# Kernel optimization log

Hardware: AMD Instinct MI355X
Metric: run time of the kernel (lower is better)

Reference implementation:

```python
import jax, jax.numpy as jnp
import numpy as np

N_NODES = 100000
N_EDGES = 400000
D_IN = 128
D_OUT = 128
BN_EPS = 1e-5


def setup_inputs() -> dict:
    key = jax.random.key(0)
    ks = jax.random.split(key, 9)
    node_feats = jax.random.normal(ks[0], (N_NODES, D_IN), dtype=jnp.float32)
    src = jax.random.randint(ks[1], (N_EDGES,), 0, N_NODES)
    dst = jax.random.randint(ks[2], (N_EDGES,), 0, N_NODES)
    # GraphConv weight/bias
    W = jax.random.normal(ks[3], (D_IN, D_OUT), dtype=jnp.float32) * (1.0 / np.sqrt(D_IN))
    b = jax.random.normal(ks[4], (D_OUT,), dtype=jnp.float32) * 0.01
    # residual Linear weight/bias
    Wr = jax.random.normal(ks[5], (D_IN, D_OUT), dtype=jnp.float32) * (1.0 / np.sqrt(D_IN))
    br = jax.random.normal(ks[6], (D_OUT,), dtype=jnp.float32) * 0.01
    # BatchNorm1d affine params
    gamma = jnp.ones((D_OUT,), dtype=jnp.float32) + 0.1 * jax.random.normal(ks[7], (D_OUT,), dtype=jnp.float32)
    beta = 0.1 * jax.random.normal(ks[8], (D_OUT,), dtype=jnp.float32)
    return {"node_feats": node_feats, "W": W, "b": b, "Wr": Wr, "br": br,
            "gamma": gamma, "beta": beta, "src": src, "dst": dst}


def reference(node_feats, W, b, Wr, br, gamma, beta, src, dst):
    ones_e = jnp.ones((src.shape[0],), dtype=node_feats.dtype)
    out_deg = jax.ops.segment_sum(ones_e, src, num_segments=N_NODES)
    in_deg = jax.ops.segment_sum(ones_e, dst, num_segments=N_NODES)
    # norm='both': D_out^{-1/2} on source side, D_in^{-1/2} on dest side (clamp 0-degree)
    c_src = jax.lax.rsqrt(jnp.maximum(out_deg, 1.0))  # [N]
    c_dst = jax.lax.rsqrt(jnp.maximum(in_deg, 1.0))   # [N]
    x_scaled = node_feats * c_src[:, None]            # [N, D_in]
    msgs = x_scaled[src]                              # gather -> [E, D_in]
    agg = jax.ops.segment_sum(msgs, dst, num_segments=N_NODES)  # scatter-add -> [N, D_in]
    h = agg * c_dst[:, None]
    h = jax.nn.relu(h @ W + b)                        # GraphConv activation
    res = jax.nn.relu(node_feats @ Wr + br)           # residual branch
    y = h + res
    # BatchNorm1d, training mode: batch stats, biased variance
    mean = jnp.mean(y, axis=0)
    var = jnp.mean(jnp.square(y - mean), axis=0)
    y_hat = (y - mean) * jax.lax.rsqrt(var + BN_EPS)
    return y_hat * gamma + beta
```

## Files before the change

kernel.cpp:

```cpp
#include <hip/hip_runtime.h>

#define N_NODES 100000
#define N_EDGES 400000
#define D 128
#define BN_EPS 1e-5f
#define NTILES 6250

typedef short short8 __attribute__((ext_vector_type(8)));
typedef float f32x4 __attribute__((ext_vector_type(4)));

static __device__ __forceinline__ float bf2f(unsigned short u) {
    unsigned x = ((unsigned)u) << 16;
    return __builtin_bit_cast(float, x);
}
static __device__ __forceinline__ unsigned short f2bf(float f) {
    unsigned x = __builtin_bit_cast(unsigned, f);
    x += 0x7fffu + ((x >> 16) & 1u);
    return (unsigned short)(x >> 16);
}
static __device__ __forceinline__ void splitbf(float a, short& hi, short& lo) {
    unsigned short h = f2bf(a);
    float r = a - bf2f(h);
    hi = (short)h;
    lo = (short)f2bf(r);
}
static __device__ __forceinline__ void split2(float a, float b, unsigned& hiw, unsigned& low) {
    short ha, la, hb, lb;
    splitbf(a, ha, la);
    splitbf(b, hb, lb);
    hiw = (unsigned)(unsigned short)ha | ((unsigned)(unsigned short)hb << 16);
    low = (unsigned)(unsigned short)la | ((unsigned)(unsigned short)lb << 16);
}
static __device__ __forceinline__ void split8(f32x4 a, f32x4 b, uint4& hi, uint4& lo) {
    unsigned h0, h1, h2, h3, l0, l1, l2, l3;
    split2(a[0], a[1], h0, l0);
    split2(a[2], a[3], h1, l1);
    split2(b[0], b[1], h2, l2);
    split2(b[2], b[3], h3, l3);
    hi = uint4{h0, h1, h2, h3};
    lo = uint4{l0, l1, l2, l3};
}

__global__ void k_zero_out(float* __restrict__ y, int n4) {
    int t = blockIdx.x * blockDim.x + threadIdx.x;
    if (t < n4) ((float4*)y)[t] = float4{0.f, 0.f, 0.f, 0.f};
}

__global__ void k_count(const int* __restrict__ src, const int* __restrict__ dst,
                        int* __restrict__ cnt_src, int* __restrict__ cnt_dst) {
    int t = blockIdx.x * blockDim.x + threadIdx.x;
    if (t >= N_EDGES) return;
    atomicAdd(&cnt_src[src[t]], 1);
    atomicAdd(&cnt_dst[dst[t]], 1);
}

__global__ void k_coeffs(const int* __restrict__ cnt_src, const int* __restrict__ cnt_dst,
                         float* __restrict__ c_src, float* __restrict__ c_dst,
                         int* __restrict__ fill) {
    int t = blockIdx.x * blockDim.x + threadIdx.x;
    if (t >= N_NODES) return;
    c_src[t] = rsqrtf(fmaxf((float)cnt_src[t], 1.0f));
    c_dst[t] = rsqrtf(fmaxf((float)cnt_dst[t], 1.0f));
    fill[t] = 0;
}

__global__ void k_scan1(const int* __restrict__ cnt, int* __restrict__ outp,
                        int* __restrict__ bsum) {
    __shared__ int s[256];
    int i = blockIdx.x * 256 + threadIdx.x;
    int v = (i < N_NODES) ? cnt[i] : 0;
    s[threadIdx.x] = v;
    __syncthreads();
    for (int d = 1; d < 256; d <<= 1) {
        int t = (threadIdx.x >= d) ? s[threadIdx.x - d] : 0;
        __syncthreads();
        s[threadIdx.x] += t;
        __syncthreads();
    }
    if (i < N_NODES) outp[i] = s[threadIdx.x] - v;
    if (threadIdx.x == 255) bsum[blockIdx.x] = s[255];
}

__global__ void k_scan2(int* __restrict__ bsum, int nb) {
    __shared__ int s[512];
    int v = (threadIdx.x < nb) ? bsum[threadIdx.x] : 0;
    s[threadIdx.x] = v;
    __syncthreads();
    for (int d = 1; d < 512; d <<= 1) {
        int t = (threadIdx.x >= d) ? s[threadIdx.x - d] : 0;
        __syncthreads();
        s[threadIdx.x] += t;
        __syncthreads();
    }
    if (threadIdx.x < nb) bsum[threadIdx.x] = s[threadIdx.x] - v;
}

__global__ void k_scan3(int* __restrict__ rowStart, const int* __restrict__ boff) {
    int i = blockIdx.x * 256 + threadIdx.x;
    if (i < N_NODES) rowStart[i] += boff[i >> 8];
    if (i == 0) rowStart[N_NODES] = N_EDGES;
}

__global__ void k_fill(const int* __restrict__ src, const int* __restrict__ dst,
                       const int* __restrict__ rowStart, int* __restrict__ fill,
                       int* __restrict__ esorted) {
    int e = blockIdx.x * blockDim.x + threadIdx.x;
    if (e >= N_EDGES) return;
    int d = dst[e];
    int pos = rowStart[d] + atomicAdd(&fill[d], 1);
    esorted[pos] = src[e];
}

__global__ void k_make_frags(const float* __restrict__ W,
                             const float* __restrict__ Wr,
                             unsigned short* __restrict__ Whi, unsigned short* __restrict__ Wlo,
                             unsigned short* __restrict__ Wrhi, unsigned short* __restrict__ Wrlo) {
    int t = blockIdx.x * blockDim.x + threadIdx.x;
    if (t >= 4096) return;
    int mat = t >> 11;
    int fragIdx = (t >> 6) & 31;
    int lane = t & 63;
    int nt = fragIdx >> 2, ks = fragIdx & 3;
    const float* Wsrc = mat ? Wr : W;
    unsigned short* dhi = mat ? Wrhi : Whi;
    unsigned short* dlo = mat ? Wrlo : Wlo;
    int n = nt * 16 + (lane & 15);
    int kbase = ks * 32 + (lane >> 4) * 8;
    short hi[8], lo[8];
#pragma unroll
    for (int j = 0; j < 8; j++) splitbf(Wsrc[(kbase + j) * D + n], hi[j], lo[j]);
    ((uint4*)dhi)[fragIdx * 64 + lane] = *(uint4*)hi;
    ((uint4*)dlo)[fragIdx * 64 + lane] = *(uint4*)lo;
}

__global__ __launch_bounds__(256, 2) void k_fused(
    const float* __restrict__ x,
    const int* __restrict__ esorted, const int* __restrict__ rowStart,
    const float* __restrict__ c_src, const float* __restrict__ c_dst,
    const unsigned short* __restrict__ Whi, const unsigned short* __restrict__ Wlo,
    const unsigned short* __restrict__ Wrhi, const unsigned short* __restrict__ Wrlo,
    const float* __restrict__ bias_h, const float* __restrict__ bias_r,
    float* __restrict__ yout,
    float* __restrict__ gsum, float* __restrict__ gsq) {
    __shared__ uint4 A[2][16][64];
    __shared__ float Y[4][16 * 36];

    const int wave = threadIdx.x >> 6;
    const int lane = threadIdx.x & 63;
    const int quad = lane >> 4;
    const int l16 = lane & 15;
    float* __restrict__ ldsY = &Y[wave][0];

    short8 wHf[8], wLf[8], rHf[8], rLf[8];
#pragma unroll
    for (int f = 0; f < 8; f++) {
        int nt = wave * 2 + (f >> 2), ks = f & 3;
        int gi = (nt * 4 + ks) * 64 + lane;
        wHf[f] = __builtin_bit_cast(short8, ((const uint4*)Whi)[gi]);
        wLf[f] = __builtin_bit_cast(short8, ((const uint4*)Wlo)[gi]);
        rHf[f] = __builtin_bit_cast(short8, ((const uint4*)Wrhi)[gi]);
        rLf[f] = __builtin_bit_cast(short8, ((const uint4*)Wrlo)[gi]);
    }
    float bh[2], brr[2];
#pragma unroll
    for (int ntl = 0; ntl < 2; ntl++) {
        int col = wave * 32 + ntl * 16 + l16;
        bh[ntl] = bias_h[col];
        brr[ntl] = bias_r[col];
    }

    float s_acc[2] = {0.f, 0.f}, q_acc[2] = {0.f, 0.f};
    const f32x4* __restrict__ xb = (const f32x4*)x;

    int buf = 0;
    for (int rt = blockIdx.x; rt < NTILES; rt += gridDim.x, buf ^= 1) {
        const int rowbase = rt * 16;

        {
            const int R = wave * 4 + quad;
            const int n = rowbase + R;
            const int li = l16;
            const int beg = rowStart[n], end = rowStart[n + 1];
            f32x4 X0 = xb[(size_t)n * 32 + li * 2], X1 = xb[(size_t)n * 32 + li * 2 + 1];
            f32x4 A0 = {0.f, 0.f, 0.f, 0.f}, A1 = {0.f, 0.f, 0.f, 0.f};
            for (int j = beg; j < end; j += 8) {
                int idx[8];
                float c[8];
                f32x4 pa[8], pb[8];
#pragma unroll
                for (int k = 0; k < 8; k++) {
                    int jj = j + k;
                    idx[k] = esorted[(jj < end) ? jj : j];
                }
#pragma unroll
                for (int k = 0; k < 8; k++)
                    c[k] = (j + k < end) ? c_src[idx[k]] : 0.f;
#pragma unroll
                for (int k = 0; k < 8; k++) {
                    pa[k] = xb[(size_t)idx[k] * 32 + li * 2];
                    pb[k] = xb[(size_t)idx[k] * 32 + li * 2 + 1];
                }
#pragma unroll
                for (int k = 0; k < 8; k++) {
                    A0 += pa[k] * c[k];
                    A1 += pb[k] * c[k];
                }
            }
            float cd = c_dst[n];
            A0 *= cd; A1 *= cd;
            uint4 ahi, alo, xhi, xlo;
            split8(A0, A1, ahi, alo);
            split8(X0, X1, xhi, xlo);
            uint4* Arow = &A[buf][R][0];
            const int sw = li ^ (R & 7);
            Arow[sw] = ahi;
            Arow[16 + sw] = alo;
            Arow[32 + sw] = xhi;
            Arow[48 + sw] = xlo;
        }
        __syncthreads();

        const uint4* rowA = &A[buf][l16][0];
        const int r7 = l16 & 7;
        short8 aH[4], aL[4], xH[4], xL[4];
#pragma unroll
        for (int ks = 0; ks < 4; ks++) {
            const int sl = (ks * 4 + quad) ^ r7;
            aH[ks] = __builtin_bit_cast(short8, rowA[sl]);
            aL[ks] = __builtin_bit_cast(short8, rowA[16 + sl]);
            xH[ks] = __builtin_bit_cast(short8, rowA[32 + sl]);
            xL[ks] = __builtin_bit_cast(short8, rowA[48 + sl]);
        }

        f32x4 accH[2], accR[2];
#pragma unroll
        for (int ntl = 0; ntl < 2; ntl++) {
            accH[ntl] = f32x4{0.f, 0.f, 0.f, 0.f};
            accR[ntl] = f32x4{0.f, 0.f, 0.f, 0.f};
#pragma unroll
            for (int ks = 0; ks < 4; ks++) {
                const int f = ntl * 4 + ks;
                accH[ntl] = __builtin_amdgcn_mfma_f32_16x16x32_bf16(aH[ks], wHf[f], accH[ntl], 0, 0, 0);
                accH[ntl] = __builtin_amdgcn_mfma_f32_16x16x32_bf16(aH[ks], wLf[f], accH[ntl], 0, 0, 0);
                accH[ntl] = __builtin_amdgcn_mfma_f32_16x16x32_bf16(aL[ks], wHf[f], accH[ntl], 0, 0, 0);
                accR[ntl] = __builtin_amdgcn_mfma_f32_16x16x32_bf16(xH[ks], rHf[f], accR[ntl], 0, 0, 0);
                accR[ntl] = __builtin_amdgcn_mfma_f32_16x16x32_bf16(xH[ks], rLf[f], accR[ntl], 0, 0, 0);
                accR[ntl] = __builtin_amdgcn_mfma_f32_16x16x32_bf16(xL[ks], rHf[f], accR[ntl], 0, 0, 0);
            }
        }

#pragma unroll
        for (int ntl = 0; ntl < 2; ntl++) {
            float s = 0.f, q = 0.f;
#pragma unroll
            for (int r = 0; r < 4; r++) {
                float y = fmaxf(accH[ntl][r] + bh[ntl], 0.f) + fmaxf(accR[ntl][r] + brr[ntl], 0.f);
                ldsY[(quad * 4 + r) * 36 + ntl * 16 + l16] = y;
                s += y;
                q += y * y;
            }
            s_acc[ntl] += s;
            q_acc[ntl] += q;
        }
        asm volatile("s_waitcnt lgkmcnt(0)");
#pragma unroll
        for (int j = 0; j < 2; j++) {
            int trow = j * 8 + (lane >> 3);
            int tc4 = lane & 7;
            float4 v = *(const float4*)&ldsY[trow * 36 + tc4 * 4];
            ((float4*)(yout + (size_t)(rowbase + trow) * D + wave * 32))[tc4] = v;
        }
    }

#pragma unroll
    for (int ntl = 0; ntl < 2; ntl++) {
        float s = s_acc[ntl], q = q_acc[ntl];
        s += __shfl_xor(s, 16, 64);
        s += __shfl_xor(s, 32, 64);
        q += __shfl_xor(q, 16, 64);
        q += __shfl_xor(q, 32, 64);
        if (lane < 16) {
            unsafeAtomicAdd(&gsum[wave * 32 + ntl * 16 + lane], s);
            unsafeAtomicAdd(&gsq[wave * 32 + ntl * 16 + lane], q);
        }
    }
}

__global__ void k_bn_stats(const float* __restrict__ gsum, const float* __restrict__ gsq,
                           const float* __restrict__ gamma, const float* __restrict__ beta,
                           float* __restrict__ scale, float* __restrict__ shift) {
    int f = threadIdx.x;
    const float invN = 1.0f / (float)N_NODES;
    float mean = gsum[f] * invN;
    float var = fmaxf(gsq[f] * invN - mean * mean, 0.f);
    float sc = gamma[f] * rsqrtf(var + BN_EPS);
    scale[f] = sc;
    shift[f] = beta[f] - mean * sc;
}

__global__ void k_bn_apply(float* __restrict__ y,
                           const float* __restrict__ scale, const float* __restrict__ shift) {
    int t = blockIdx.x * blockDim.x + threadIdx.x;
    const int total4 = N_NODES * D / 4;
    if (t >= total4) return;
    float4 v = ((float4*)y)[t];
    int f = (t * 4) & (D - 1);
    v.x = v.x * scale[f] + shift[f];
    v.y = v.y * scale[f + 1] + shift[f + 1];
    v.z = v.z * scale[f + 2] + shift[f + 2];
    v.w = v.w * scale[f + 3] + shift[f + 3];
    ((float4*)y)[t] = v;
}

extern "C" void kernel_launch(void* const* d_in, const int* in_sizes, int n_in,
                              void* d_out, int out_size, void* d_ws, size_t ws_size,
                              hipStream_t stream) {
    const float* x     = (const float*)d_in[0];
    const float* W     = (const float*)d_in[1];
    const float* b     = (const float*)d_in[2];
    const float* Wr    = (const float*)d_in[3];
    const float* br    = (const float*)d_in[4];
    const float* gamma = (const float*)d_in[5];
    const float* beta  = (const float*)d_in[6];
    const int* src = (const int*)d_in[7];
    const int* dst = (const int*)d_in[8];
    float* out = (float*)d_out;

    const int NB1 = (N_NODES + 255) / 256;

    char* ws = (char*)d_ws;
    size_t off = 0;
    float* gsum    = (float*)(ws + off); off += 512;
    float* gsq     = (float*)(ws + off); off += 512;
    int* cnt_src   = (int*)(ws + off); off += 400128;
    int* cnt_dst   = (int*)(ws + off); off += 400128;
    const size_t zero_bytes = off;
    int* fill      = (int*)(ws + off); off += 400128;
    int* rowStart  = (int*)(ws + off); off += 400384;
    int* bsum      = (int*)(ws + off); off += 2048;
    int* esorted   = (int*)(ws + off); off += (size_t)N_EDGES * 4;
    float* c_src   = (float*)(ws + off); off += 400128;
    float* c_dst   = (float*)(ws + off); off += 400128;
    unsigned short* WhiF  = (unsigned short*)(ws + off); off += 32768;
    unsigned short* WloF  = (unsigned short*)(ws + off); off += 32768;
    unsigned short* WrhiF = (unsigned short*)(ws + off); off += 32768;
    unsigned short* WrloF = (unsigned short*)(ws + off); off += 32768;
    float* scale = (float*)(ws + off); off += 512;
    float* shift = (float*)(ws + off); off += 512;
    const size_t needed = off;

    if (ws_size < needed) {
        k_zero_out<<<(N_NODES * D / 4 + 255) / 256, 256, 0, stream>>>(out, N_NODES * D / 4);
        return;
    }

    hipMemsetAsync(d_ws, 0, zero_bytes, stream);

    k_make_frags<<<16, 256, 0, stream>>>(W, Wr, WhiF, WloF, WrhiF, WrloF);
    k_count<<<(N_EDGES + 255) / 256, 256, 0, stream>>>(src, dst, cnt_src, cnt_dst);
    k_coeffs<<<NB1, 256, 0, stream>>>(cnt_src, cnt_dst, c_src, c_dst, fill);
    k_scan1<<<NB1, 256, 0, stream>>>(cnt_dst, rowStart, bsum);
    k_scan2<<<1, 512, 0, stream>>>(bsum, NB1);
    k_scan3<<<NB1, 256, 0, stream>>>(rowStart, bsum);
    k_fill<<<(N_EDGES + 255) / 256, 256, 0, stream>>>(src, dst, rowStart, fill, esorted);
    k_fused<<<1024, 256, 0, stream>>>(x, esorted, rowStart, c_src, c_dst,
                                      WhiF, WloF, WrhiF, WrloF, b, br, out, gsum, gsq);
    k_bn_stats<<<1, 128, 0, stream>>>(gsum, gsq, gamma, beta, scale, shift);
    k_bn_apply<<<(N_NODES * D / 4 + 255) / 256, 256, 0, stream>>>(out, scale, shift);
}
```

Before: 250.5 us.

## Software-pipeline gather under MFMA and fold BatchNorm into cooperative kernel

Restructures the fused kernel so each tile's neighbour gather for the next row tile is issued in stages between the GraphConv and residual MFMA blocks. This hides global-load latency behind matrix math. The BN statistics and apply steps move into the same kernel behind a cooperative grid sync, which removes two launches but halves the grid to 512 blocks and re-reads the output. The coefficient kernel is also merged into the first scan pass. The cooperative launch needs a fallback path, and the smaller grid may lower occupancy for the gather.

```diff
diff --git a/kernel.cpp b/kernel.cpp
--- a/kernel.cpp
+++ b/kernel.cpp
@@ -1,10 +1,12 @@
 #include <hip/hip_runtime.h>
+#include <hip/hip_cooperative_groups.h>
 
 #define N_NODES 100000
 #define N_EDGES 400000
 #define D 128
 #define BN_EPS 1e-5f
 #define NTILES 6250
+#define COOP_GRID 512
 
 typedef short short8 __attribute__((ext_vector_type(8)));
 typedef float f32x4 __attribute__((ext_vector_type(4)));
@@ -54,21 +56,19 @@
     atomicAdd(&cnt_dst[dst[t]], 1);
 }
 
-__global__ void k_coeffs(const int* __restrict__ cnt_src, const int* __restrict__ cnt_dst,
-                         float* __restrict__ c_src, float* __restrict__ c_dst,
-                         int* __restrict__ fill) {
-    int t = blockIdx.x * blockDim.x + threadIdx.x;
-    if (t >= N_NODES) return;
-    c_src[t] = rsqrtf(fmaxf((float)cnt_src[t], 1.0f));
-    c_dst[t] = rsqrtf(fmaxf((float)cnt_dst[t], 1.0f));
-    fill[t] = 0;
-}
-
 __global__ void k_scan1(const int* __restrict__ cnt, int* __restrict__ outp,
-                        int* __restrict__ bsum) {
+                        int* __restrict__ bsum,
+                        const int* __restrict__ cnt_src,
+                        float* __restrict__ c_src, float* __restrict__ c_dst,
+                        int* __restrict__ fill) {
     __shared__ int s[256];
     int i = blockIdx.x * 256 + threadIdx.x;
     int v = (i < N_NODES) ? cnt[i] : 0;
+    if (i < N_NODES) {
+        c_src[i] = rsqrtf(fmaxf((float)cnt_src[i], 1.0f));
+        c_dst[i] = rsqrtf(fmaxf((float)v, 1.0f));
+        fill[i] = 0;
+    }
     s[threadIdx.x] = v;
     __syncthreads();
     for (int d = 1; d < 256; d <<= 1) {
@@ -141,15 +141,21 @@
     const unsigned short* __restrict__ Wrhi, const unsigned short* __restrict__ Wrlo,
     const float* __restrict__ bias_h, const float* __restrict__ bias_r,
     float* __restrict__ yout,
-    float* __restrict__ gsum, float* __restrict__ gsq) {
+    float* __restrict__ gsum, float* __restrict__ gsq,
+    const float* __restrict__ gamma, const float* __restrict__ beta,
+    int coop) {
     __shared__ uint4 A[2][16][64];
     __shared__ float Y[4][16 * 36];
+    __shared__ float sc[128], sh[128];
 
     const int wave = threadIdx.x >> 6;
     const int lane = threadIdx.x & 63;
     const int quad = lane >> 4;
     const int l16 = lane & 15;
+    const int R = wave * 4 + quad;
+    const int li = l16;
     float* __restrict__ ldsY = &Y[wave][0];
+    const f32x4* __restrict__ xb = (const f32x4*)x;
 
     short8 wHf[8], wLf[8], rHf[8], rLf[8];
 #pragma unroll
@@ -170,55 +176,64 @@
     }
 
     float s_acc[2] = {0.f, 0.f}, q_acc[2] = {0.f, 0.f};
-    const f32x4* __restrict__ xb = (const f32x4*)x;
+    const int rt0 = blockIdx.x;
+    const int G = gridDim.x;
+
+    {
+        const int n = rt0 * 16 + R;
+        const int beg = rowStart[n], end = rowStart[n + 1];
+        f32x4 X0 = xb[(size_t)n * 32 + li * 2], X1 = xb[(size_t)n * 32 + li * 2 + 1];
+        f32x4 A0 = {0.f, 0.f, 0.f, 0.f}, A1 = {0.f, 0.f, 0.f, 0.f};
+        for (int j = beg; j < end; j += 8) {
+            int idx[8]; float c[8]; f32x4 pa[8], pb[8];
+#pragma unroll
+            for (int k = 0; k < 8; k++) {
+                int jj = j + k;
+                idx[k] = esorted[(jj < end) ? jj : j];
+            }
+#pragma unroll
+            for (int k = 0; k < 8; k++) c[k] = (j + k < end) ? c_src[idx[k]] : 0.f;
+#pragma unroll
+            for (int k = 0; k < 8; k++) {
+                pa[k] = xb[(size_t)idx[k] * 32 + li * 2];
+                pb[k] = xb[(size_t)idx[k] * 32 + li * 2 + 1];
+            }
+#pragma unroll
+            for (int k = 0; k < 8; k++) { A0 += pa[k] * c[k]; A1 += pb[k] * c[k]; }
+        }
+        float cd = c_dst[n];
+        A0 *= cd; A1 *= cd;
+        uint4 ahi, alo, xhi, xlo;
+        split8(A0, A1, ahi, alo);
+        split8(X0, X1, xhi, xlo);
+        uint4* Arow = &A[0][R][0];
+        const int sw = li ^ (R & 7);
+        Arow[sw] = ahi; Arow[16 + sw] = alo; Arow[32 + sw] = xhi; Arow[48 + sw] = xlo;
+    }
+    int beg1 = 0, end1 = 0;
+    if (rt0 + G < NTILES) {
+        int n1 = (rt0 + G) * 16 + R;
+        beg1 = rowStart[n1];
+        end1 = rowStart[n1 + 1];
+    }
 
     int buf = 0;
-    for (int rt = blockIdx.x; rt < NTILES; rt += gridDim.x, buf ^= 1) {
+    for (int rt = rt0; rt < NTILES; rt += G, buf ^= 1) {
         const int rowbase = rt * 16;
-
-        {
-            const int R = wave * 4 + quad;
-            const int n = rowbase + R;
-            const int li = l16;
-            const int beg = rowStart[n], end = rowStart[n + 1];
-            f32x4 X0 = xb[(size_t)n * 32 + li * 2], X1 = xb[(size_t)n * 32 + li * 2 + 1];
-            f32x4 A0 = {0.f, 0.f, 0.f, 0.f}, A1 = {0.f, 0.f, 0.f, 0.f};
-            for (int j = beg; j < end; j += 8) {
-                int idx[8];
-                float c[8];
-                f32x4 pa[8], pb[8];
-#pragma unroll
-                for (int k = 0; k < 8; k++) {
-                    int jj = j + k;
-                    idx[k] = esorted[(jj < end) ? jj : j];
-                }
-#pragma unroll
-                for (int k = 0; k < 8; k++)
-                    c[k] = (j + k < end) ? c_src[idx[k]] : 0.f;
-#pragma unroll
-                for (int k = 0; k < 8; k++) {
-                    pa[k] = xb[(size_t)idx[k] * 32 + li * 2];
-                    pb[k] = xb[(size_t)idx[k] * 32 + li * 2 + 1];
-                }
-#pragma unroll
-                for (int k = 0; k < 8; k++) {
-                    A0 += pa[k] * c[k];
-                    A1 += pb[k] * c[k];
-                }
-            }
-            float cd = c_dst[n];
-            A0 *= cd; A1 *= cd;
-            uint4 ahi, alo, xhi, xlo;
-            split8(A0, A1, ahi, alo);
-            split8(X0, X1, xhi, xlo);
-            uint4* Arow = &A[buf][R][0];
-            const int sw = li ^ (R & 7);
-            Arow[sw] = ahi;
-            Arow[16 + sw] = alo;
-            Arow[32 + sw] = xhi;
-            Arow[48 + sw] = xlo;
-        }
-        __syncthreads();
+        const int rtn = rt + G;
+        const bool pf = rtn < NTILES;
+        const int n1 = rtn * 16 + R;
+
+        __syncthreads();
+
+        int idx[8];
+        if (pf) {
+#pragma unroll
+            for (int k = 0; k < 8; k++) {
+                int jj = beg1 + k;
+                idx[k] = esorted[(jj < end1) ? jj : beg1];
+            }
+        }
 
         const uint4* rowA = &A[buf][l16][0];
         const int r7 = l16 & 7;
@@ -236,17 +251,42 @@
 #pragma unroll
         for (int ntl = 0; ntl < 2; ntl++) {
             accH[ntl] = f32x4{0.f, 0.f, 0.f, 0.f};
-            accR[ntl] = f32x4{0.f, 0.f, 0.f, 0.f};
 #pragma unroll
             for (int ks = 0; ks < 4; ks++) {
                 const int f = ntl * 4 + ks;
                 accH[ntl] = __builtin_amdgcn_mfma_f32_16x16x32_bf16(aH[ks], wHf[f], accH[ntl], 0, 0, 0);
                 accH[ntl] = __builtin_amdgcn_mfma_f32_16x16x32_bf16(aH[ks], wLf[f], accH[ntl], 0, 0, 0);
                 accH[ntl] = __builtin_amdgcn_mfma_f32_16x16x32_bf16(aL[ks], wHf[f], accH[ntl], 0, 0, 0);
+            }
+        }
+
+        float c[8];
+        if (pf) {
+#pragma unroll
+            for (int k = 0; k < 8; k++) c[k] = (beg1 + k < end1) ? c_src[idx[k]] : 0.f;
+        }
+
+#pragma unroll
+        for (int ntl = 0; ntl < 2; ntl++) {
+            accR[ntl] = f32x4{0.f, 0.f, 0.f, 0.f};
+#pragma unroll
+            for (int ks = 0; ks < 4; ks++) {
+                const int f = ntl * 4 + ks;
                 accR[ntl] = __builtin_amdgcn_mfma_f32_16x16x32_bf16(xH[ks], rHf[f], accR[ntl], 0, 0, 0);
                 accR[ntl] = __builtin_amdgcn_mfma_f32_16x16x32_bf16(xH[ks], rLf[f], accR[ntl], 0, 0, 0);
                 accR[ntl] = __builtin_amdgcn_mfma_f32_16x16x32_bf16(xL[ks], rHf[f], accR[ntl], 0, 0, 0);
             }
+        }
+
+        f32x4 pa[8], pb[8], X0n, X1n;
+        if (pf) {
+#pragma unroll
+            for (int k = 0; k < 8; k++) {
+                pa[k] = xb[(size_t)idx[k] * 32 + li * 2];
+                pb[k] = xb[(size_t)idx[k] * 32 + li * 2 + 1];
+            }
+            X0n = xb[(size_t)n1 * 32 + li * 2];
+            X1n = xb[(size_t)n1 * 32 + li * 2 + 1];
         }
 
 #pragma unroll
@@ -269,6 +309,43 @@
             int tc4 = lane & 7;
             float4 v = *(const float4*)&ldsY[trow * 36 + tc4 * 4];
             ((float4*)(yout + (size_t)(rowbase + trow) * D + wave * 32))[tc4] = v;
+        }
+
+        if (pf) {
+            f32x4 A0 = {0.f, 0.f, 0.f, 0.f}, A1 = {0.f, 0.f, 0.f, 0.f};
+#pragma unroll
+            for (int k = 0; k < 8; k++) { A0 += pa[k] * c[k]; A1 += pb[k] * c[k]; }
+            for (int j = beg1 + 8; j < end1; j += 8) {
+                int idx2[8]; float c2[8]; f32x4 qa[8], qb[8];
+#pragma unroll
+                for (int k = 0; k < 8; k++) {
+                    int jj = j + k;
+                    idx2[k] = esorted[(jj < end1) ? jj : j];
+                }
+#pragma unroll
+                for (int k = 0; k < 8; k++) c2[k] = (j + k < end1) ? c_src[idx2[k]] : 0.f;
+#pragma unroll
+                for (int k = 0; k < 8; k++) {
+                    qa[k] = xb[(size_t)idx2[k] * 32 + li * 2];
+                    qb[k] = xb[(size_t)idx2[k] * 32 + li * 2 + 1];
+                }
+#pragma unroll
+                for (int k = 0; k < 8; k++) { A0 += qa[k] * c2[k]; A1 += qb[k] * c2[k]; }
+            }
+            float cd = c_dst[n1];
+            A0 *= cd; A1 *= cd;
+            uint4 ahi, alo, xhi, xlo;
+            split8(A0, A1, ahi, alo);
+            split8(X0n, X1n, xhi, xlo);
+            uint4* Arow = &A[buf ^ 1][R][0];
+            const int sw = li ^ (R & 7);
+            Arow[sw] = ahi; Arow[16 + sw] = alo; Arow[32 + sw] = xhi; Arow[48 + sw] = xlo;
+            int rt2 = rtn + G;
+            if (rt2 < NTILES) {
+                int n2 = rt2 * 16 + R;
+                beg1 = rowStart[n2];
+                end1 = rowStart[n2 + 1];
+            }
         }
     }
 
@@ -282,6 +359,32 @@
         if (lane < 16) {
             unsafeAtomicAdd(&gsum[wave * 32 + ntl * 16 + lane], s);
             unsafeAtomicAdd(&gsq[wave * 32 + ntl * 16 + lane], q);
+        }
+    }
+
+    if (coop) {
+        cooperative_groups::this_grid().sync();
+        if (threadIdx.x < 128) {
+            int f = threadIdx.x;
+            float s = __hip_atomic_load(&gsum[f], __ATOMIC_RELAXED, __HIP_MEMORY_SCOPE_AGENT);
+            float q = __hip_atomic_load(&gsq[f], __ATOMIC_RELAXED, __HIP_MEMORY_SCOPE_AGENT);
+            const float invN = 1.0f / (float)N_NODES;
+            float mean = s * invN;
+            float var = fmaxf(q * invN - mean * mean, 0.f);
+            float scl = gamma[f] * rsqrtf(var + BN_EPS);
+            sc[f] = scl;
+            sh[f] = beta[f] - mean * scl;
+        }
+        __syncthreads();
+        const int total4 = N_NODES * D / 4;
+        for (int i = blockIdx.x * blockDim.x + threadIdx.x; i < total4; i += gridDim.x * blockDim.x) {
+            float4 v = ((float4*)yout)[i];
+            int f = (i * 4) & (D - 1);
+            v.x = v.x * sc[f] + sh[f];
+            v.y = v.y * sc[f + 1] + sh[f + 1];
+            v.z = v.z * sc[f + 2] + sh[f + 2];
+            v.w = v.w * sc[f + 3] + sh[f + 3];
+            ((float4*)yout)[i] = v;
         }
     }
 }
@@ -358,13 +461,26 @@
 
     k_make_frags<<<16, 256, 0, stream>>>(W, Wr, WhiF, WloF, WrhiF, WrloF);
     k_count<<<(N_EDGES + 255) / 256, 256, 0, stream>>>(src, dst, cnt_src, cnt_dst);
-    k_coeffs<<<NB1, 256, 0, stream>>>(cnt_src, cnt_dst, c_src, c_dst, fill);
-    k_scan1<<<NB1, 256, 0, stream>>>(cnt_dst, rowStart, bsum);
+    k_scan1<<<NB1, 256, 0, stream>>>(cnt_dst, rowStart, bsum, cnt_src, c_src, c_dst, fill);
     k_scan2<<<1, 512, 0, stream>>>(bsum, NB1);
     k_scan3<<<NB1, 256, 0, stream>>>(rowStart, bsum);
     k_fill<<<(N_EDGES + 255) / 256, 256, 0, stream>>>(src, dst, rowStart, fill, esorted);
-    k_fused<<<1024, 256, 0, stream>>>(x, esorted, rowStart, c_src, c_dst,
-                                      WhiF, WloF, WrhiF, WrloF, b, br, out, gsum, gsq);
-    k_bn_stats<<<1, 128, 0, stream>>>(gsum, gsq, gamma, beta, scale, shift);
-    k_bn_apply<<<(N_NODES * D / 4 + 255) / 256, 256, 0, stream>>>(out, scale, shift);
-}
+
+    int coopFlag = 1;
+    void* kargs[] = {
+        (void*)&x, (void*)&esorted, (void*)&rowStart, (void*)&c_src, (void*)&c_dst,
+        (void*)&WhiF, (void*)&WloF, (void*)&WrhiF, (void*)&WrloF,
+        (void*)&b, (void*)&br, (void*)&out, (void*)&gsum, (void*)&gsq,
+        (void*)&gamma, (void*)&beta, (void*)&coopFlag
+    };
+    hipError_t ce = hipLaunchCooperativeKernel((const void*)k_fused, dim3(COOP_GRID), dim3(256),
+                                               kargs, 0, stream);
+    if (ce != hipSuccess) {
+        (void)hipGetLastError();
+        k_fused<<<1024, 256, 0, stream>>>(x, esorted, rowStart, c_src, c_dst,
+                                          WhiF, WloF, WrhiF, WrloF, b, br, out,
+                                          gsum, gsq, gamma, beta, 0);
+        k_bn_stats<<<1, 128, 0, stream>>>(gsum, gsq, gamma, beta, scale, shift);
+        k_bn_apply<<<(N_NODES * D / 4 + 255) / 256, 256, 0, stream>>>(out, scale, shift);
+    }
+}
```

Result: slower. 456.7 us (+82.3%).
